# Optimization experiments

Hardware: AMD Instinct MI355X
Metric: run time of the kernel (lower is better)

## Reference

```python
import jax, jax.numpy as jnp
import numpy as np

OUTPUT_SIZE = (7, 7)
SPATIAL_SCALE = 0.0625
B, C, H, W = 4, 256, 38, 38
N_ROIS = 512
IMG = int(W / SPATIAL_SCALE)  # 608


def setup_inputs() -> dict:
    key = jax.random.key(0)
    k_feat, k_bidx, k_xy = jax.random.split(key, 3)
    features = jax.random.normal(k_feat, (B, C, H, W), dtype=jnp.float32)
    batch_idx = jax.random.randint(k_bidx, (N_ROIS, 1), 0, B).astype(jnp.float32)
    # (x1,x2) and (y1,y2) sampled in image coords, sorted so x1<=x2, y1<=y2
    xy = jax.random.uniform(k_xy, (N_ROIS, 2, 2), minval=0.0, maxval=float(IMG))
    xy = jnp.sort(xy, axis=2)  # [N, {x,y}, {lo,hi}]
    rois = jnp.concatenate(
        [batch_idx, xy[:, 0, 0:1], xy[:, 1, 0:1], xy[:, 0, 1:2], xy[:, 1, 1:2]],
        axis=1,
    ).astype(jnp.float32)  # [N,5] = (b, x1, y1, x2, y2)
    return {"features": features, "rois": rois}


def _roi_pool(features, rois, output_size, spatial_scale):
    Ph, Pw = output_size
    Bf, Cf, Hf, Wf = features.shape
    bidx = rois[:, 0].astype(jnp.int32)
    # torch .long() truncates toward zero; coords are non-negative here
    coords = jnp.trunc(rois[:, 1:5] * spatial_scale).astype(jnp.int32)
    x1 = jnp.clip(coords[:, 0], 0, Wf - 1)
    y1 = jnp.clip(coords[:, 1], 0, Hf - 1)
    x2 = jnp.clip(coords[:, 2], 0, Wf - 1)
    y2 = jnp.clip(coords[:, 3], 0, Hf - 1)
    hh = y2 - y1 + 1  # region height (inclusive slice y1:y2+1)
    ww = x2 - x1 + 1
    feat = features[bidx]  # [N,C,H,W] per-ROI gathered feature map
    hs = jnp.arange(Hf)
    ws = jnp.arange(Wf)
    NEG = jnp.finfo(features.dtype).min
    # adaptive_max_pool2d bins: start = floor(p*size/P), end = ceil((p+1)*size/P)
    # 2D max over a rectangle = max over rows then max over cols.
    rows = []
    for p in range(Ph):
        s = y1 + (p * hh) // Ph
        e = y1 + ((p + 1) * hh + Ph - 1) // Ph  # ceil div
        m = (hs[None, :] >= s[:, None]) & (hs[None, :] < e[:, None])  # [N,H]
        rows.append(jnp.max(jnp.where(m[:, None, :, None], feat, NEG), axis=2))  # [N,C,W]
    ry = jnp.stack(rows, axis=2)  # [N,C,Ph,W]
    cols = []
    for q in range(Pw):
        s = x1 + (q * ww) // Pw
        e = x1 + ((q + 1) * ww + Pw - 1) // Pw
        m = (ws[None, :] >= s[:, None]) & (ws[None, :] < e[:, None])  # [N,W]
        cols.append(jnp.max(jnp.where(m[:, None, None, :], ry, NEG), axis=3))  # [N,C,Ph]
    return jnp.stack(cols, axis=3)  # [N,C,Ph,Pw]


def reference(features, rois):
    return _roi_pool(features, rois, OUTPUT_SIZE, SPATIAL_SCALE)
```

## Files before the change

### kernel.cpp

```cpp
#include <hip/hip_runtime.h>


#define NROIS 512
#define CCH   256
#define FH    38
#define FW    38
#define HW    (FH * FW)
#define SCALE 0.0625f
#define NEGF  (-3.402823466e+38f)

__global__ __launch_bounds__(256) void transpose_kernel(
    const float* __restrict__ src, float* __restrict__ dst)
{
    __shared__ float tile[4][257];
    const int b  = blockIdx.y;
    const int s0 = blockIdx.x * 4;
    const int t  = threadIdx.x;

    const float4 v = *(const float4*)(src + ((size_t)(b * CCH + t)) * HW + s0);
    tile[0][t] = v.x; tile[1][t] = v.y; tile[2][t] = v.z; tile[3][t] = v.w;
    __syncthreads();

    const int s = t >> 6;
    const int m = t & 63;
    float* drow = dst + ((size_t)b * HW + s0 + s) * CCH;
    #pragma unroll
    for (int k = 0; k < 4; ++k)
        drow[m + 64 * k] = tile[s][m + 64 * k];
}

template <int WW>
__device__ __forceinline__ void load_row(float (&v)[WW], const float* __restrict__ rb)
{
    #pragma unroll
    for (int j = 0; j < WW; ++j) v[j] = rb[j * CCH];
}

template <int WW>
__device__ __forceinline__ void consume_row(const float (&v)[WW], float (&acc)[7])
{
    #pragma unroll
    for (int q = 0; q < 7; ++q) {
        const int xs = (q * WW) / 7;
        const int xe = ((q + 1) * WW + 6) / 7;
        #pragma unroll
        for (int j = xs; j < xe; ++j)
            acc[q] = fmaxf(acc[q], v[j]);
    }
}

template <int WW>
__device__ __forceinline__ void pool_p_row(
    const float* __restrict__ rb0,
    int h,
    float (&acc)[7])
{
    if constexpr (WW <= 18) {
        float va[WW], vb[WW];
        load_row<WW>(va, rb0);
        for (int y = 0; y < h; y += 2) {
            const float* r1 = rb0 + (size_t)min(y + 1, h - 1) * (FW * CCH);
            load_row<WW>(vb, r1);
            consume_row<WW>(va, acc);
            const float* r2 = rb0 + (size_t)min(y + 2, h - 1) * (FW * CCH);
            load_row<WW>(va, r2);
            consume_row<WW>(vb, acc);
        }
    } else {
        const float* rb = rb0;
        for (int y = 0; y < h; ++y) {
            float v[WW];
            load_row<WW>(v, rb);
            consume_row<WW>(v, acc);
            rb += (size_t)FW * CCH;
        }
    }
}

template <int NB>
__device__ __forceinline__ void write_out(
    float* __restrict__ outb, const float (*__restrict__ sm)[65], int tid)
{
    #pragma unroll
    for (int flat = 0; flat < 64 * NB; flat += 256) {
        const int f = flat + tid;
        if (f < 64 * NB) {
            const int c = f / NB;
            const int l = f - c * NB;
            outb[c * 49 + l] = sm[l][c];
        }
    }
}

__global__ __launch_bounds__(256) void roipool_kernel(
    const float* __restrict__ featT,
    const float* __restrict__ rois,
    float* __restrict__ out)
{
    __shared__ float smem[28][65];

    const int n    = blockIdx.y;
    const int cg   = blockIdx.x * 64;
    const int ph   = blockIdx.z;
    const int tid  = threadIdx.x;
    const int wv   = __builtin_amdgcn_readfirstlane(tid >> 6);
    const int lane = tid & 63;
    const int p    = wv + 4 * ph;

    const float* r = rois + n * 5;
    const int b = (int)r[0];
    int x1 = (int)(r[1] * SCALE);
    int y1 = (int)(r[2] * SCALE);
    int x2 = (int)(r[3] * SCALE);
    int y2 = (int)(r[4] * SCALE);
    x1 = min(max(x1, 0), FW - 1);
    y1 = min(max(y1, 0), FH - 1);
    x2 = min(max(x2, 0), FW - 1);
    y2 = min(max(y2, 0), FH - 1);
    const int hh = y2 - y1 + 1;
    const int ww = x2 - x1 + 1;

    if (p < 7) {
        const int ys = y1 + (p * hh) / 7;
        const int h  = (y1 + ((p + 1) * hh + 6) / 7) - ys;

        const float* rb0 = featT + (size_t)b * HW * CCH + cg + lane
                         + (size_t)(ys * FW + x1) * CCH;

        float acc[7];
        #pragma unroll
        for (int q = 0; q < 7; ++q) acc[q] = NEGF;

        switch (ww) {
            case  1: pool_p_row< 1>(rb0, h, acc); break;
            case  2: pool_p_row< 2>(rb0, h, acc); break;
            case  3: pool_p_row< 3>(rb0, h, acc); break;
            case  4: pool_p_row< 4>(rb0, h, acc); break;
            case  5: pool_p_row< 5>(rb0, h, acc); break;
            case  6: pool_p_row< 6>(rb0, h, acc); break;
            case  7: pool_p_row< 7>(rb0, h, acc); break;
            case  8: pool_p_row< 8>(rb0, h, acc); break;
            case  9: pool_p_row< 9>(rb0, h, acc); break;
            case 10: pool_p_row<10>(rb0, h, acc); break;
            case 11: pool_p_row<11>(rb0, h, acc); break;
            case 12: pool_p_row<12>(rb0, h, acc); break;
            case 13: pool_p_row<13>(rb0, h, acc); break;
            case 14: pool_p_row<14>(rb0, h, acc); break;
            case 15: pool_p_row<15>(rb0, h, acc); break;
            case 16: pool_p_row<16>(rb0, h, acc); break;
            case 17: pool_p_row<17>(rb0, h, acc); break;
            case 18: pool_p_row<18>(rb0, h, acc); break;
            case 19: pool_p_row<19>(rb0, h, acc); break;
            case 20: pool_p_row<20>(rb0, h, acc); break;
            case 21: pool_p_row<21>(rb0, h, acc); break;
            case 22: pool_p_row<22>(rb0, h, acc); break;
            case 23: pool_p_row<23>(rb0, h, acc); break;
            case 24: pool_p_row<24>(rb0, h, acc); break;
            case 25: pool_p_row<25>(rb0, h, acc); break;
            case 26: pool_p_row<26>(rb0, h, acc); break;
            case 27: pool_p_row<27>(rb0, h, acc); break;
            case 28: pool_p_row<28>(rb0, h, acc); break;
            case 29: pool_p_row<29>(rb0, h, acc); break;
            case 30: pool_p_row<30>(rb0, h, acc); break;
            case 31: pool_p_row<31>(rb0, h, acc); break;
            case 32: pool_p_row<32>(rb0, h, acc); break;
            case 33: pool_p_row<33>(rb0, h, acc); break;
            case 34: pool_p_row<34>(rb0, h, acc); break;
            case 35: pool_p_row<35>(rb0, h, acc); break;
            case 36: pool_p_row<36>(rb0, h, acc); break;
            case 37: pool_p_row<37>(rb0, h, acc); break;
            default: pool_p_row<38>(rb0, h, acc); break;
        }

        #pragma unroll
        for (int q = 0; q < 7; ++q)
            smem[wv * 7 + q][lane] = acc[q];
    }
    __syncthreads();

    float* outb = out + (size_t)n * (CCH * 49) + (size_t)cg * 49 + ph * 28;
    if (ph == 0) write_out<28>(outb, smem, tid);
    else         write_out<21>(outb, smem, tid);
}

__global__ __launch_bounds__(256) void roipool_fallback(
    const float* __restrict__ feat,
    const float* __restrict__ rois,
    float* __restrict__ out)
{
    int idx = blockIdx.x * blockDim.x + threadIdx.x;
    int q = idx % 7;
    int t = idx / 7;
    int p = t % 7;
    t /= 7;
    int c = t % CCH;
    int n = t / CCH;

    const float* r = rois + n * 5;
    int b  = (int)r[0];
    int x1 = (int)(r[1] * SCALE);
    int y1 = (int)(r[2] * SCALE);
    int x2 = (int)(r[3] * SCALE);
    int y2 = (int)(r[4] * SCALE);
    x1 = min(max(x1, 0), FW - 1);
    y1 = min(max(y1, 0), FH - 1);
    x2 = min(max(x2, 0), FW - 1);
    y2 = min(max(y2, 0), FH - 1);
    int hh = y2 - y1 + 1, ww = x2 - x1 + 1;

    int ys = y1 + (p * hh) / 7, ye = y1 + ((p + 1) * hh + 6) / 7;
    int xs = x1 + (q * ww) / 7, xe = x1 + ((q + 1) * ww + 6) / 7;

    const float* base = feat + ((size_t)b * CCH + c) * HW;
    float m = NEGF;
    for (int y = ys; y < ye; ++y)
        for (int x = xs; x < xe; ++x)
            m = fmaxf(m, base[y * FW + x]);
    out[idx] = m;
}

extern "C" void kernel_launch(void* const* d_in, const int* in_sizes, int n_in,
                              void* d_out, int out_size, void* d_ws, size_t ws_size,
                              hipStream_t stream) {
    const float* feat = (const float*)d_in[0];
    const float* rois = (const float*)d_in[1];
    float* out = (float*)d_out;

    const size_t need = (size_t)4 * HW * CCH * sizeof(float);
    if (ws_size < need) {
        const int total = NROIS * CCH * 49;
        roipool_fallback<<<(total + 255) / 256, 256, 0, stream>>>(feat, rois, out);
        return;
    }

    float* featT = (float*)d_ws;

    dim3 tg(HW / 4, 4);
    transpose_kernel<<<tg, 256, 0, stream>>>(feat, featT);

    dim3 pg(4, NROIS, 2);
    roipool_kernel<<<pg, 256, 0, stream>>>(featT, rois, out);
}
```

Measured before the change: 27.83 us.

## Bucket ROIs by image and map each image to an XCD pair for L2 locality

The transpose kernel now also counting-sorts ROIs by batch index into a permutation with per-image counts and offsets. The pooling kernel becomes a 4096-block grid-stride loop in which the block index modulo 8 picks an XCD, so each image's ROIs are processed on two XCDs. This is meant to keep each image's transposed feature map in a smaller set of L2 caches. It also drops the double-buffered row loads for narrow ROIs, adds extra syncs per unit, and relies on round-robin block-to-XCD dispatch, which can leave load imbalanced if images have unequal ROI counts.

```diff
diff --git a/kernel.cpp b/kernel.cpp
--- a/kernel.cpp
+++ b/kernel.cpp
@@ -9,10 +9,16 @@
 #define SCALE 0.0625f
 #define NEGF  (-3.402823466e+38f)
 
-__global__ __launch_bounds__(256) void transpose_kernel(
-    const float* __restrict__ src, float* __restrict__ dst)
+#define FEATT_BYTES ((size_t)4 * HW * CCH * sizeof(float))
+
+__global__ __launch_bounds__(256) void transpose_bucket_kernel(
+    const float* __restrict__ src, const float* __restrict__ rois,
+    float* __restrict__ dst, int* __restrict__ perm,
+    int* __restrict__ cntG, int* __restrict__ offG)
 {
     __shared__ float tile[4][257];
+    __shared__ int cntS[4], baseS[4];
+
     const int b  = blockIdx.y;
     const int s0 = blockIdx.x * 4;
     const int t  = threadIdx.x;
@@ -27,53 +33,48 @@
     #pragma unroll
     for (int k = 0; k < 4; ++k)
         drow[m + 64 * k] = tile[s][m + 64 * k];
+
+    if (blockIdx.x == 0 && blockIdx.y == 0) {
+        if (t < 4) cntS[t] = 0;
+        __syncthreads();
+        const int b0 = (int)rois[t * 5];
+        const int p0 = atomicAdd(&cntS[b0], 1);
+        const int b1 = (int)rois[(t + 256) * 5];
+        const int p1 = atomicAdd(&cntS[b1], 1);
+        __syncthreads();
+        if (t == 0) {
+            int acc = 0;
+            #pragma unroll
+            for (int i = 0; i < 4; ++i) {
+                baseS[i] = acc;
+                cntG[i] = cntS[i];
+                offG[i] = acc;
+                acc += cntS[i];
+            }
+        }
+        __syncthreads();
+        perm[baseS[b0] + p0] = t;
+        perm[baseS[b1] + p1] = t + 256;
+    }
 }
 
 template <int WW>
-__device__ __forceinline__ void load_row(float (&v)[WW], const float* __restrict__ rb)
-{
-    #pragma unroll
-    for (int j = 0; j < WW; ++j) v[j] = rb[j * CCH];
-}
-
-template <int WW>
-__device__ __forceinline__ void consume_row(const float (&v)[WW], float (&acc)[7])
-{
-    #pragma unroll
-    for (int q = 0; q < 7; ++q) {
-        const int xs = (q * WW) / 7;
-        const int xe = ((q + 1) * WW + 6) / 7;
+__device__ __forceinline__ void pool_one(
+    const float* __restrict__ rb, int h, float (&acc)[7])
+{
+    for (int y = 0; y < h; ++y) {
+        float v[WW];
         #pragma unroll
-        for (int j = xs; j < xe; ++j)
-            acc[q] = fmaxf(acc[q], v[j]);
-    }
-}
-
-template <int WW>
-__device__ __forceinline__ void pool_p_row(
-    const float* __restrict__ rb0,
-    int h,
-    float (&acc)[7])
-{
-    if constexpr (WW <= 18) {
-        float va[WW], vb[WW];
-        load_row<WW>(va, rb0);
-        for (int y = 0; y < h; y += 2) {
-            const float* r1 = rb0 + (size_t)min(y + 1, h - 1) * (FW * CCH);
-            load_row<WW>(vb, r1);
-            consume_row<WW>(va, acc);
-            const float* r2 = rb0 + (size_t)min(y + 2, h - 1) * (FW * CCH);
-            load_row<WW>(va, r2);
-            consume_row<WW>(vb, acc);
-        }
-    } else {
-        const float* rb = rb0;
-        for (int y = 0; y < h; ++y) {
-            float v[WW];
-            load_row<WW>(v, rb);
-            consume_row<WW>(v, acc);
-            rb += (size_t)FW * CCH;
-        }
+        for (int j = 0; j < WW; ++j) v[j] = rb[j * CCH];
+        #pragma unroll
+        for (int q = 0; q < 7; ++q) {
+            const int xs = (q * WW) / 7;
+            const int xe = ((q + 1) * WW + 6) / 7;
+            #pragma unroll
+            for (int j = xs; j < xe; ++j)
+                acc[q] = fmaxf(acc[q], v[j]);
+        }
+        rb += (size_t)FW * CCH;
     }
 }
 
@@ -95,92 +96,109 @@
 __global__ __launch_bounds__(256) void roipool_kernel(
     const float* __restrict__ featT,
     const float* __restrict__ rois,
+    const int* __restrict__ perm,
+    const int* __restrict__ cntG,
+    const int* __restrict__ offG,
     float* __restrict__ out)
 {
     __shared__ float smem[28][65];
 
-    const int n    = blockIdx.y;
-    const int cg   = blockIdx.x * 64;
-    const int ph   = blockIdx.z;
+    const int bid  = blockIdx.x;
+    const int xcd  = bid & 7;
+    const int slot = bid >> 3;
+    const int img  = xcd >> 1;
+    const int half = xcd & 1;
     const int tid  = threadIdx.x;
     const int wv   = __builtin_amdgcn_readfirstlane(tid >> 6);
     const int lane = tid & 63;
-    const int p    = wv + 4 * ph;
-
-    const float* r = rois + n * 5;
-    const int b = (int)r[0];
-    int x1 = (int)(r[1] * SCALE);
-    int y1 = (int)(r[2] * SCALE);
-    int x2 = (int)(r[3] * SCALE);
-    int y2 = (int)(r[4] * SCALE);
-    x1 = min(max(x1, 0), FW - 1);
-    y1 = min(max(y1, 0), FH - 1);
-    x2 = min(max(x2, 0), FW - 1);
-    y2 = min(max(y2, 0), FH - 1);
-    const int hh = y2 - y1 + 1;
-    const int ww = x2 - x1 + 1;
-
-    if (p < 7) {
-        const int ys = y1 + (p * hh) / 7;
-        const int h  = (y1 + ((p + 1) * hh + 6) / 7) - ys;
-
-        const float* rb0 = featT + (size_t)b * HW * CCH + cg + lane
-                         + (size_t)(ys * FW + x1) * CCH;
-
-        float acc[7];
-        #pragma unroll
-        for (int q = 0; q < 7; ++q) acc[q] = NEGF;
-
-        switch (ww) {
-            case  1: pool_p_row< 1>(rb0, h, acc); break;
-            case  2: pool_p_row< 2>(rb0, h, acc); break;
-            case  3: pool_p_row< 3>(rb0, h, acc); break;
-            case  4: pool_p_row< 4>(rb0, h, acc); break;
-            case  5: pool_p_row< 5>(rb0, h, acc); break;
-            case  6: pool_p_row< 6>(rb0, h, acc); break;
-            case  7: pool_p_row< 7>(rb0, h, acc); break;
-            case  8: pool_p_row< 8>(rb0, h, acc); break;
-            case  9: pool_p_row< 9>(rb0, h, acc); break;
-            case 10: pool_p_row<10>(rb0, h, acc); break;
-            case 11: pool_p_row<11>(rb0, h, acc); break;
-            case 12: pool_p_row<12>(rb0, h, acc); break;
-            case 13: pool_p_row<13>(rb0, h, acc); break;
-            case 14: pool_p_row<14>(rb0, h, acc); break;
-            case 15: pool_p_row<15>(rb0, h, acc); break;
-            case 16: pool_p_row<16>(rb0, h, acc); break;
-            case 17: pool_p_row<17>(rb0, h, acc); break;
-            case 18: pool_p_row<18>(rb0, h, acc); break;
-            case 19: pool_p_row<19>(rb0, h, acc); break;
-            case 20: pool_p_row<20>(rb0, h, acc); break;
-            case 21: pool_p_row<21>(rb0, h, acc); break;
-            case 22: pool_p_row<22>(rb0, h, acc); break;
-            case 23: pool_p_row<23>(rb0, h, acc); break;
-            case 24: pool_p_row<24>(rb0, h, acc); break;
-            case 25: pool_p_row<25>(rb0, h, acc); break;
-            case 26: pool_p_row<26>(rb0, h, acc); break;
-            case 27: pool_p_row<27>(rb0, h, acc); break;
-            case 28: pool_p_row<28>(rb0, h, acc); break;
-            case 29: pool_p_row<29>(rb0, h, acc); break;
-            case 30: pool_p_row<30>(rb0, h, acc); break;
-            case 31: pool_p_row<31>(rb0, h, acc); break;
-            case 32: pool_p_row<32>(rb0, h, acc); break;
-            case 33: pool_p_row<33>(rb0, h, acc); break;
-            case 34: pool_p_row<34>(rb0, h, acc); break;
-            case 35: pool_p_row<35>(rb0, h, acc); break;
-            case 36: pool_p_row<36>(rb0, h, acc); break;
-            case 37: pool_p_row<37>(rb0, h, acc); break;
-            default: pool_p_row<38>(rb0, h, acc); break;
-        }
-
-        #pragma unroll
-        for (int q = 0; q < 7; ++q)
-            smem[wv * 7 + q][lane] = acc[q];
-    }
-    __syncthreads();
-
-    float* outb = out + (size_t)n * (CCH * 49) + (size_t)cg * 49 + ph * 28;
-    if (ph == 0) write_out<28>(outb, smem, tid);
-    else         write_out<21>(outb, smem, tid);
+
+    const int cnt = cntG[img];
+    const int off = offG[img];
+    const int nunits = cnt * 8;
+
+    for (int g = slot * 2 + half; g < nunits; g += 1024) {
+        const int r  = perm[off + (g >> 3)];
+        const int u  = g & 7;
+        const int cg = u & 3;
+        const int ph = u >> 2;
+
+        const float* rr = rois + r * 5;
+        const int bb = (int)rr[0];
+        int x1 = (int)(rr[1] * SCALE);
+        int y1 = (int)(rr[2] * SCALE);
+        int x2 = (int)(rr[3] * SCALE);
+        int y2 = (int)(rr[4] * SCALE);
+        x1 = min(max(x1, 0), FW - 1);
+        y1 = min(max(y1, 0), FH - 1);
+        x2 = min(max(x2, 0), FW - 1);
+        y2 = min(max(y2, 0), FH - 1);
+        const int hh = y2 - y1 + 1;
+        const int ww = x2 - x1 + 1;
+
+        const int p = 4 * ph + wv;
+        if (p < 7) {
+            const int ys = y1 + (p * hh) / 7;
+            const int h  = (y1 + ((p + 1) * hh + 6) / 7) - ys;
+
+            const float* rb0 = featT + (size_t)bb * HW * CCH + cg * 64 + lane
+                             + (size_t)(ys * FW + x1) * CCH;
+
+            float acc[7];
+            #pragma unroll
+            for (int q = 0; q < 7; ++q) acc[q] = NEGF;
+
+            switch (ww) {
+                case  1: pool_one< 1>(rb0, h, acc); break;
+                case  2: pool_one< 2>(rb0, h, acc); break;
+                case  3: pool_one< 3>(rb0, h, acc); break;
+                case  4: pool_one< 4>(rb0, h, acc); break;
+                case  5: pool_one< 5>(rb0, h, acc); break;
+                case  6: pool_one< 6>(rb0, h, acc); break;
+                case  7: pool_one< 7>(rb0, h, acc); break;
+                case  8: pool_one< 8>(rb0, h, acc); break;
+                case  9: pool_one< 9>(rb0, h, acc); break;
+                case 10: pool_one<10>(rb0, h, acc); break;
+                case 11: pool_one<11>(rb0, h, acc); break;
+                case 12: pool_one<12>(rb0, h, acc); break;
+                case 13: pool_one<13>(rb0, h, acc); break;
+                case 14: pool_one<14>(rb0, h, acc); break;
+                case 15: pool_one<15>(rb0, h, acc); break;
+                case 16: pool_one<16>(rb0, h, acc); break;
+                case 17: pool_one<17>(rb0, h, acc); break;
+                case 18: pool_one<18>(rb0, h, acc); break;
+                case 19: pool_one<19>(rb0, h, acc); break;
+                case 20: pool_one<20>(rb0, h, acc); break;
+                case 21: pool_one<21>(rb0, h, acc); break;
+                case 22: pool_one<22>(rb0, h, acc); break;
+                case 23: pool_one<23>(rb0, h, acc); break;
+                case 24: pool_one<24>(rb0, h, acc); break;
+                case 25: pool_one<25>(rb0, h, acc); break;
+                case 26: pool_one<26>(rb0, h, acc); break;
+                case 27: pool_one<27>(rb0, h, acc); break;
+                case 28: pool_one<28>(rb0, h, acc); break;
+                case 29: pool_one<29>(rb0, h, acc); break;
+                case 30: pool_one<30>(rb0, h, acc); break;
+                case 31: pool_one<31>(rb0, h, acc); break;
+                case 32: pool_one<32>(rb0, h, acc); break;
+                case 33: pool_one<33>(rb0, h, acc); break;
+                case 34: pool_one<34>(rb0, h, acc); break;
+                case 35: pool_one<35>(rb0, h, acc); break;
+                case 36: pool_one<36>(rb0, h, acc); break;
+                case 37: pool_one<37>(rb0, h, acc); break;
+                default: pool_one<38>(rb0, h, acc); break;
+            }
+
+            #pragma unroll
+            for (int q = 0; q < 7; ++q)
+                smem[wv * 7 + q][lane] = acc[q];
+        }
+        __syncthreads();
+
+        float* outb = out + (size_t)r * (CCH * 49) + cg * (64 * 49) + ph * 28;
+        if (ph == 0) write_out<28>(outb, smem, tid);
+        else         write_out<21>(outb, smem, tid);
+        __syncthreads();
+    }
 }
 
 __global__ __launch_bounds__(256) void roipool_fallback(
@@ -226,7 +244,7 @@
     const float* rois = (const float*)d_in[1];
     float* out = (float*)d_out;
 
-    const size_t need = (size_t)4 * HW * CCH * sizeof(float);
+    const size_t need = FEATT_BYTES + (NROIS + 8) * sizeof(int);
     if (ws_size < need) {
         const int total = NROIS * CCH * 49;
         roipool_fallback<<<(total + 255) / 256, 256, 0, stream>>>(feat, rois, out);
@@ -234,10 +252,13 @@
     }
 
     float* featT = (float*)d_ws;
+    int*   perm  = (int*)((char*)d_ws + FEATT_BYTES);
+    int*   cntG  = perm + NROIS;
+    int*   offG  = cntG + 4;
 
     dim3 tg(HW / 4, 4);
-    transpose_kernel<<<tg, 256, 0, stream>>>(feat, featT);
-
-    dim3 pg(4, NROIS, 2);
-    roipool_kernel<<<pg, 256, 0, stream>>>(featT, rois, out);
-}
+    transpose_bucket_kernel<<<tg, 256, 0, stream>>>(feat, rois, featT,
+                                                    perm, cntG, offG);
+
+    roipool_kernel<<<4096, 256, 0, stream>>>(featT, rois, perm, cntG, offG, out);
+}
```

Result: slower. 30.32 us (+8.9%).
